# Optimization experiments

Measured on AMD Instinct MI355X. Metric: run time of the kernel, lower is better.

## Reference

```python
import jax, jax.numpy as jnp
import numpy as np

NUM_SENT, SENT_LEN, HIDDEN, OUT = 128, 64, 512, 512
N = NUM_SENT * SENT_LEN


def setup_inputs() -> dict:
    key = jax.random.key(0)
    ks = jax.random.split(key, 14)
    s = 1.0 / np.sqrt(HIDDEN)
    so = 1.0 / np.sqrt(OUT)
    return {
        "x": jax.random.normal(ks[0], (NUM_SENT, SENT_LEN, HIDDEN), jnp.float32),
        "mask": jax.random.uniform(ks[1], (N,), jnp.float32),
        "a_ud": jax.random.normal(ks[2], (N, N), jnp.float32) * 0.01,
        "a_lr": jax.random.normal(ks[3], (N, N), jnp.float32) * 0.01,
        "W": jax.random.uniform(ks[4], (OUT, HIDDEN), jnp.float32, -s, s),
        "b": jax.random.uniform(ks[5], (OUT,), jnp.float32, -s, s),
        "W_ud": jax.random.uniform(ks[6], (OUT, HIDDEN), jnp.float32, -s, s),
        "b_ud": jax.random.uniform(ks[7], (OUT,), jnp.float32, -s, s),
        "W_lr": jax.random.uniform(ks[8], (OUT, HIDDEN), jnp.float32, -s, s),
        "b_lr": jax.random.uniform(ks[9], (OUT,), jnp.float32, -s, s),
        "W_g": jax.random.uniform(ks[10], (OUT, HIDDEN), jnp.float32, -s, s),
        "b_g": jax.random.uniform(ks[11], (OUT,), jnp.float32, -s, s),
        "W_go": jax.random.uniform(ks[12], (OUT, OUT), jnp.float32, -so, so),
        "b_go": jax.random.uniform(ks[13], (OUT,), jnp.float32, -so, so),
    }


def reference(x, mask, a_ud, a_lr, W, b, W_ud, b_ud, W_lr, b_lr, W_g, b_g, W_go, b_go):
    num_sent, sent_len, hidden = x.shape
    xf = x.reshape(-1, hidden)                       # [N, H]
    h_ud = a_ud @ xf                                 # [N, H] neighbor aggregation (up/down)
    h_lr = a_lr @ xf                                 # [N, H] neighbor aggregation (left/right)
    h = (xf @ W.T + b) + (h_ud @ W_ud.T + b_ud) + (h_lr @ W_lr.T + b_lr)  # [N, OUT]
    # global node branch: masked mean-pool of relu(linear_g(x))
    n = mask.sum()
    h_g = (mask[None, :] @ jax.nn.relu(xf @ W_g.T + b_g)) / n  # [1, OUT]
    h = h + (h_g @ W_go.T + b_go)                    # broadcast add over N rows
    h = jax.nn.relu(h).reshape(num_sent, sent_len, -1)
    return (h, h_g)
```

## Files before the change

### kernel.cpp

```cpp
#include <hip/hip_runtime.h>
#include <stdint.h>


typedef __attribute__((ext_vector_type(8))) short short8;
typedef __attribute__((ext_vector_type(4))) float f32x4;

typedef const __attribute__((address_space(1))) void* gas1_t;
typedef __attribute__((address_space(3))) void* las3_t;

__device__ __forceinline__ void gload16(const void* g, void* l) {
  __builtin_amdgcn_global_load_lds((gas1_t)g, (las3_t)l, 16, 0, 0);
}

__device__ __forceinline__ unsigned pack2t(float lo, float hi) {
  return __builtin_amdgcn_perm(__float_as_uint(hi), __float_as_uint(lo), 0x07060302u);
}

__device__ __forceinline__ unsigned f2bf_rne(float f) {
  unsigned u = __float_as_uint(f);
  return (u + 0x7FFFu + ((u >> 16) & 1u)) >> 16;
}
__device__ __forceinline__ unsigned pack2_rne(float lo, float hi) {
  return f2bf_rne(lo) | (f2bf_rne(hi) << 16);
}

__global__ __launch_bounds__(256) void k1_convert(
    const float* __restrict__ x, const float* __restrict__ W,
    const float* __restrict__ W_ud, const float* __restrict__ W_lr,
    const float* __restrict__ W_g,
    uint16_t* __restrict__ xb, uint16_t* __restrict__ Yt, uint16_t* __restrict__ Wb1)
{
  unsigned tid = blockIdx.x * 256u + threadIdx.x;
  const float* src;
  uint16_t* dst;
  if (tid < 524288u) {
    src = x + (size_t)tid * 8;
    dst = xb + (size_t)tid * 8;
  } else {
    unsigned r = tid - 524288u;
    unsigned which = r >> 15;
    unsigned e8 = (r & 32767u) * 8;
    src = (which == 0 ? W : which == 1 ? W_ud : which == 2 ? W_lr : W_g) + e8;
    if (which == 0) {
      unsigned n = e8 >> 9, k = e8 & 511u;
      dst = Yt + (size_t)n * 16896 + 16384 + k;
    } else {
      dst = Wb1 + (size_t)(which - 1) * 262144 + e8;
    }
  }
  float4 v0 = ((const float4*)src)[0];
  float4 v1 = ((const float4*)src)[1];
  uint4 p;
  p.x = pack2_rne(v0.x, v0.y); p.y = pack2_rne(v0.z, v0.w);
  p.z = pack2_rne(v1.x, v1.y); p.w = pack2_rne(v1.z, v1.w);
  *(uint4*)dst = p;
}

__global__ __launch_bounds__(256) void k2_gemm1(
    const uint16_t* __restrict__ xb, const uint16_t* __restrict__ Wb1,
    const float* __restrict__ mask, const float* __restrict__ b_g,
    uint16_t* __restrict__ Yt, float* __restrict__ colsum)
{
  __shared__ __align__(16) char smem[34816];
  char* const bufA = smem;
  char* const bufB = smem + 8192;

  const int t = threadIdx.x;
  const int i0 = blockIdx.x * 128;
  const int bn = blockIdx.y;
  const int n0 = bn * 128;
  const int lane = t & 63, w = t >> 6;
  const int q = lane >> 4, l15 = lane & 15;
  const int wm = w >> 1, wn = w & 1;
  const int srow = t >> 2, spart = t & 3;

  f32x4 acc[4][4] = {};

  const uint16_t* const aA0 = xb + (size_t)(i0 + srow) * 512 + spart * 8;
  const uint16_t* const aA1 = aA0 + (size_t)64 * 512;
  const uint16_t* const aB0 = Wb1 + (size_t)(n0 + srow) * 512 + spart * 8;
  const uint16_t* const aB1 = aB0 + (size_t)64 * 512;

  for (int s = 0; s < 16; ++s) {
    __syncthreads();
    const int kk = s << 5;
    gload16(aA0 + kk, bufA + t * 16);
    gload16(aA1 + kk, bufA + 4096 + t * 16);
    gload16(aB0 + kk, bufB + t * 16);
    gload16(aB1 + kk, bufB + 4096 + t * 16);
    __syncthreads();
    short8 af[4], bf[4];
#pragma unroll
    for (int mi = 0; mi < 4; ++mi)
      af[mi] = *(const short8*)(bufA + (wm * 64 + mi * 16 + l15) * 64 + q * 16);
#pragma unroll
    for (int ni = 0; ni < 4; ++ni)
      bf[ni] = *(const short8*)(bufB + (wn * 64 + ni * 16 + l15) * 64 + q * 16);
#pragma unroll
    for (int mi = 0; mi < 4; ++mi)
#pragma unroll
      for (int ni = 0; ni < 4; ++ni)
        acc[mi][ni] = __builtin_amdgcn_mfma_f32_16x16x32_bf16(af[mi], bf[ni], acc[mi][ni], 0, 0, 0);
  }
  __syncthreads();

  const int g = bn >> 2;
  const int jb = (bn & 3) * 128;

  if (g < 2) {
    uint16_t* T = (uint16_t*)smem;
#pragma unroll
    for (int mi = 0; mi < 4; ++mi) {
#pragma unroll
      for (int ni = 0; ni < 4; ++ni) {
        int jl = wn * 64 + ni * 16 + l15;
#pragma unroll
        for (int r = 0; r < 4; ++r) {
          int il = wm * 64 + mi * 16 + q * 4 + r;
          T[jl * 136 + il] = (uint16_t)f2bf_rne(acc[mi][ni][r]);
        }
      }
    }
    __syncthreads();
    const int jl = t >> 1, half = t & 1;
    uint16_t* dst = Yt + (size_t)(jb + jl) * 16896 + (size_t)g * 8192 + i0 + half * 64;
    const uint16_t* srcT = T + jl * 136 + half * 64;
#pragma unroll
    for (int c = 0; c < 8; ++c)
      *(uint4*)(dst + c * 8) = *(const uint4*)(srcT + c * 8);
  } else {
    float mk[4][4];
#pragma unroll
    for (int mi = 0; mi < 4; ++mi)
#pragma unroll
      for (int r = 0; r < 4; ++r)
        mk[mi][r] = mask[i0 + wm * 64 + mi * 16 + q * 4 + r];
#pragma unroll
    for (int ni = 0; ni < 4; ++ni) {
      const int jl = jb + wn * 64 + ni * 16 + l15;
      const float bg = b_g[jl];
      float p = 0.f;
#pragma unroll
      for (int mi = 0; mi < 4; ++mi)
#pragma unroll
        for (int r = 0; r < 4; ++r)
          p += fmaxf(acc[mi][ni][r] + bg, 0.f) * mk[mi][r];
      p += __shfl_xor(p, 16);
      p += __shfl_xor(p, 32);
      if (q == 0) atomicAdd(&colsum[jl], p);
    }
  }
}

__global__ __launch_bounds__(256) void k4_finalize(
    const float* __restrict__ colsum, const float* __restrict__ mask,
    const float* __restrict__ b, const float* __restrict__ b_ud,
    const float* __restrict__ b_lr, const float* __restrict__ W_go,
    const float* __restrict__ b_go,
    float* __restrict__ row_add, float* __restrict__ out_hg)
{
  __shared__ float red[256];
  __shared__ float hg[512];
  const int t = threadIdx.x;
  float s = 0.f;
  for (int k = t; k < 8192; k += 256) s += mask[k];
  red[t] = s;
  __syncthreads();
  for (int o = 128; o > 0; o >>= 1) {
    if (t < o) red[t] += red[t + o];
    __syncthreads();
  }
  const float n = red[0];
  for (int j = t; j < 512; j += 256) hg[j] = colsum[j] / n;
  __syncthreads();

  const int j0 = blockIdx.x * 64;
  const int jj = j0 + (t >> 2);
  const int seg = t & 3;
  const float4* wrow = (const float4*)(W_go + (size_t)jj * 512 + seg * 128);
  float p = 0.f;
#pragma unroll 4
  for (int c = 0; c < 32; ++c) {
    float4 wv = wrow[c];
    const float* h4 = &hg[seg * 128 + c * 4];
    p += wv.x * h4[0] + wv.y * h4[1] + wv.z * h4[2] + wv.w * h4[3];
  }
  p += __shfl_down(p, 2);
  p += __shfl_down(p, 1);
  if ((t & 3) == 0)
    row_add[jj] = b[jj] + b_ud[jj] + b_lr[jj] + b_go[jj] + p;
  if (t < 64) out_hg[j0 + t] = hg[j0 + t];
}

__global__ __launch_bounds__(256, 4) void k5_gemm_big(
    const float* __restrict__ a_ud, const float* __restrict__ a_lr,
    const float* __restrict__ x, const uint16_t* __restrict__ Yt,
    float* __restrict__ out, float* __restrict__ P, int nsteps)
{
  __shared__ __align__(16) char smem[34816];
  char* const A0 = smem;
  char* const A1 = smem + 9216;
  char* const B0 = smem + 18432;
  char* const B1 = smem + 26624;

  const int t = threadIdx.x;
  const int i0 = blockIdx.x * 128;
  const int j0 = blockIdx.y * 128;
  const int z  = blockIdx.z;
  const int lane = t & 63;
  const int q = lane >> 4, l15 = lane & 15;
  const int w = t >> 6;
  const int wm = w >> 1, wn = w & 1;

  const int arow = t >> 1, ahalf = t & 1;
  const int brow = t >> 2;
  const int bchunk = (t & 3) ^ ((t >> 3) & 3);

  f32x4 acc[4][4] = {};
  const int kbase0 = z * (nsteps << 5);

  float4 av0, av1, av2, av3;
#define A_SRC(gk) ((gk) < 8192 \
    ? a_ud + (size_t)(i0 + arow) * 8192 + (gk) + ahalf * 16 \
    : ((gk) < 16384 \
      ? a_lr + (size_t)(i0 + arow) * 8192 + ((gk) - 8192) + ahalf * 16 \
      : x + (size_t)(i0 + arow) * 512 + ((gk) - 16384) + ahalf * 16))

  {
    const float* as = A_SRC(kbase0);
    av0 = ((const float4*)as)[0]; av1 = ((const float4*)as)[1];
    av2 = ((const float4*)as)[2]; av3 = ((const float4*)as)[3];
#pragma unroll
    for (int r = 0; r < 2; ++r)
      gload16(Yt + (size_t)(j0 + brow + r * 64) * 16896 + kbase0 + bchunk * 8,
              B0 + r * 4096 + t * 16);
    uint4 p0, p1;
    p0.x = pack2t(av0.x, av0.y); p0.y = pack2t(av0.z, av0.w);
    p0.z = pack2t(av1.x, av1.y); p0.w = pack2t(av1.z, av1.w);
    p1.x = pack2t(av2.x, av2.y); p1.y = pack2t(av2.z, av2.w);
    p1.z = pack2t(av3.x, av3.y); p1.w = pack2t(av3.z, av3.w);
    *(uint4*)(A0 + arow * 72 + ahalf * 32) = p0;
    *(uint4*)(A0 + arow * 72 + ahalf * 32 + 16) = p1;
  }

  for (int s = 0; s < nsteps; ++s) {
    __syncthreads();
    const bool more = (s + 1 < nsteps);
    char* const cA = (s & 1) ? A1 : A0;
    char* const cB = (s & 1) ? B1 : B0;
    char* const nA = (s & 1) ? A0 : A1;
    char* const nB = (s & 1) ? B0 : B1;

    if (more) {
      const int gk = kbase0 + ((s + 1) << 5);
      const float* as = A_SRC(gk);
      av0 = ((const float4*)as)[0]; av1 = ((const float4*)as)[1];
      av2 = ((const float4*)as)[2]; av3 = ((const float4*)as)[3];
#pragma unroll
      for (int r = 0; r < 2; ++r)
        gload16(Yt + (size_t)(j0 + brow + r * 64) * 16896 + gk + bchunk * 8,
                nB + r * 4096 + t * 16);
    }

    short8 af[4], bf[4];
#pragma unroll
    for (int mi = 0; mi < 4; ++mi)
      af[mi] = *(const short8*)(cA + (wm * 64 + mi * 16 + l15) * 72 + q * 16);
#pragma unroll
    for (int ni = 0; ni < 4; ++ni) {
      const int j = wn * 64 + ni * 16 + l15;
      bf[ni] = *(const short8*)(cB + j * 64 + ((q ^ ((j >> 1) & 3)) * 16));
    }
#pragma unroll
    for (int mi = 0; mi < 4; ++mi)
#pragma unroll
      for (int ni = 0; ni < 4; ++ni)
        acc[mi][ni] = __builtin_amdgcn_mfma_f32_16x16x32_bf16(af[mi], bf[ni], acc[mi][ni], 0, 0, 0);

    if (more) {
      uint4 p0, p1;
      p0.x = pack2t(av0.x, av0.y); p0.y = pack2t(av0.z, av0.w);
      p0.z = pack2t(av1.x, av1.y); p0.w = pack2t(av1.z, av1.w);
      p1.x = pack2t(av2.x, av2.y); p1.y = pack2t(av2.z, av2.w);
      p1.z = pack2t(av3.x, av3.y); p1.w = pack2t(av3.z, av3.w);
      *(uint4*)(nA + arow * 72 + ahalf * 32) = p0;
      *(uint4*)(nA + arow * 72 + ahalf * 32 + 16) = p1;
    }
  }
#undef A_SRC

  float* dst = z ? P + (size_t)(z - 1) * 4194304 : out;
#pragma unroll
  for (int ni = 0; ni < 4; ++ni) {
    const int jl = j0 + wn * 64 + ni * 16 + l15;
#pragma unroll
    for (int mi = 0; mi < 4; ++mi)
#pragma unroll
      for (int r = 0; r < 4; ++r) {
        const int il = i0 + wm * 64 + mi * 16 + q * 4 + r;
        dst[(size_t)il * 512 + jl] = acc[mi][ni][r];
      }
  }
}

__global__ __launch_bounds__(256) void k6_combine(
    const float* __restrict__ P, const float* __restrict__ row_add,
    float* __restrict__ out, int npart)
{
  const int idx = blockIdx.x * 256 + threadIdx.x;
  float4 a = ((const float4*)out)[idx];
  for (int p = 0; p < npart; ++p) {
    const float4 v = ((const float4*)P)[(size_t)p * 1048576 + idx];
    a.x += v.x; a.y += v.y; a.z += v.z; a.w += v.w;
  }
  const float4 r = ((const float4*)row_add)[idx & 127];
  float4 o;
  o.x = fmaxf(a.x + r.x, 0.f);
  o.y = fmaxf(a.y + r.y, 0.f);
  o.z = fmaxf(a.z + r.z, 0.f);
  o.w = fmaxf(a.w + r.w, 0.f);
  ((float4*)out)[idx] = o;
}

extern "C" void kernel_launch(void* const* d_in, const int* in_sizes, int n_in,
                              void* d_out, int out_size, void* d_ws, size_t ws_size,
                              hipStream_t stream) {
  (void)in_sizes; (void)n_in; (void)out_size;
  const float* x    = (const float*)d_in[0];
  const float* mask = (const float*)d_in[1];
  const float* a_ud = (const float*)d_in[2];
  const float* a_lr = (const float*)d_in[3];
  const float* W    = (const float*)d_in[4];
  const float* b    = (const float*)d_in[5];
  const float* W_ud = (const float*)d_in[6];
  const float* b_ud = (const float*)d_in[7];
  const float* W_lr = (const float*)d_in[8];
  const float* b_lr = (const float*)d_in[9];
  const float* W_g  = (const float*)d_in[10];
  const float* b_g  = (const float*)d_in[11];
  const float* W_go = (const float*)d_in[12];
  const float* b_go = (const float*)d_in[13];
  float* out = (float*)d_out;

  char* ws = (char*)d_ws;
  uint16_t* xb     = (uint16_t*)(ws);
  uint16_t* Yt     = (uint16_t*)(ws + 8388608);
  uint16_t* Wb1    = (uint16_t*)(ws + 25690112);
  float*    colsum = (float*)(ws + 27262976);
  float*    rowadd = (float*)(ws + 27265024);
  float*    P      = (float*)(ws + 27267072);

  const int Z = (ws_size >= 77598720u) ? 4 : 2;
  const int nsteps = (16896 / Z) / 32;

  hipMemsetAsync(colsum, 0, 512 * sizeof(float), stream);
  k1_convert<<<2560, 256, 0, stream>>>(x, W, W_ud, W_lr, W_g, xb, Yt, Wb1);
  k2_gemm1<<<dim3(64, 12), 256, 0, stream>>>(xb, Wb1, mask, b_g, Yt, colsum);
  k4_finalize<<<8, 256, 0, stream>>>(colsum, mask, b, b_ud, b_lr, W_go, b_go,
                                     rowadd, out + 4194304);
  k5_gemm_big<<<dim3(64, 4, Z), 256, 0, stream>>>(a_ud, a_lr, x, Yt, out, P, nsteps);
  k6_combine<<<4096, 256, 0, stream>>>(P, rowadd, out, Z - 1);
}
```

Measured before the change: 863.0 us.

## Double-buffer gemm1 with swizzled LDS and deepen big-GEMM A prefetch to two stages

In the first GEMM kernel, tiles are now double-buffered in LDS and prefetched one step ahead. An XOR swizzle on the chunk index is meant to cut LDS bank conflicts, and one barrier per step is removed. In the big GEMM, the fp32 A operand now loads two steps ahead into alternating register sets, with explicit vmcnt waits and sched_barriers replacing __syncthreads, to hide global latency more deeply. The big GEMM's occupancy hint drops from 4 to 3 blocks per SIMD to allow the extra registers. This loses some latency hiding from fewer resident waves, and the hand-written waitcnt counts must match the number of outstanding loads exactly.

```diff
diff --git a/kernel.cpp b/kernel.cpp
--- a/kernel.cpp
+++ b/kernel.cpp
@@ -62,8 +62,10 @@
     uint16_t* __restrict__ Yt, float* __restrict__ colsum)
 {
   __shared__ __align__(16) char smem[34816];
-  char* const bufA = smem;
-  char* const bufB = smem + 8192;
+  char* const A0 = smem;
+  char* const B0 = smem + 8192;
+  char* const A1 = smem + 16384;
+  char* const B1 = smem + 24576;
 
   const int t = threadIdx.x;
   const int i0 = blockIdx.x * 128;
@@ -72,30 +74,45 @@
   const int lane = t & 63, w = t >> 6;
   const int q = lane >> 4, l15 = lane & 15;
   const int wm = w >> 1, wn = w & 1;
-  const int srow = t >> 2, spart = t & 3;
+  const int srow = t >> 2;
+  const int sw = (t & 3) ^ ((srow >> 1) & 3);
 
   f32x4 acc[4][4] = {};
 
-  const uint16_t* const aA0 = xb + (size_t)(i0 + srow) * 512 + spart * 8;
+  const uint16_t* const aA0 = xb + (size_t)(i0 + srow) * 512 + sw * 8;
   const uint16_t* const aA1 = aA0 + (size_t)64 * 512;
-  const uint16_t* const aB0 = Wb1 + (size_t)(n0 + srow) * 512 + spart * 8;
+  const uint16_t* const aB0 = Wb1 + (size_t)(n0 + srow) * 512 + sw * 8;
   const uint16_t* const aB1 = aB0 + (size_t)64 * 512;
+
+  gload16(aA0, A0 + t * 16);
+  gload16(aA1, A0 + 4096 + t * 16);
+  gload16(aB0, B0 + t * 16);
+  gload16(aB1, B0 + 4096 + t * 16);
 
   for (int s = 0; s < 16; ++s) {
     __syncthreads();
-    const int kk = s << 5;
-    gload16(aA0 + kk, bufA + t * 16);
-    gload16(aA1 + kk, bufA + 4096 + t * 16);
-    gload16(aB0 + kk, bufB + t * 16);
-    gload16(aB1 + kk, bufB + 4096 + t * 16);
-    __syncthreads();
+    if (s < 15) {
+      const int kk = (s + 1) << 5;
+      char* const nA = (s & 1) ? A0 : A1;
+      char* const nB = (s & 1) ? B0 : B1;
+      gload16(aA0 + kk, nA + t * 16);
+      gload16(aA1 + kk, nA + 4096 + t * 16);
+      gload16(aB0 + kk, nB + t * 16);
+      gload16(aB1 + kk, nB + 4096 + t * 16);
+    }
+    char* const cA = (s & 1) ? A1 : A0;
+    char* const cB = (s & 1) ? B1 : B0;
     short8 af[4], bf[4];
 #pragma unroll
-    for (int mi = 0; mi < 4; ++mi)
-      af[mi] = *(const short8*)(bufA + (wm * 64 + mi * 16 + l15) * 64 + q * 16);
-#pragma unroll
-    for (int ni = 0; ni < 4; ++ni)
-      bf[ni] = *(const short8*)(bufB + (wn * 64 + ni * 16 + l15) * 64 + q * 16);
+    for (int mi = 0; mi < 4; ++mi) {
+      const int r = wm * 64 + mi * 16 + l15;
+      af[mi] = *(const short8*)(cA + r * 64 + ((q ^ ((r >> 1) & 3)) * 16));
+    }
+#pragma unroll
+    for (int ni = 0; ni < 4; ++ni) {
+      const int r = wn * 64 + ni * 16 + l15;
+      bf[ni] = *(const short8*)(cB + r * 64 + ((q ^ ((r >> 1) & 3)) * 16));
+    }
 #pragma unroll
     for (int mi = 0; mi < 4; ++mi)
 #pragma unroll
@@ -192,7 +209,7 @@
   if (t < 64) out_hg[j0 + t] = hg[j0 + t];
 }
 
-__global__ __launch_bounds__(256, 4) void k5_gemm_big(
+__global__ __launch_bounds__(256, 3) void k5_gemm_big(
     const float* __restrict__ a_ud, const float* __restrict__ a_lr,
     const float* __restrict__ x, const uint16_t* __restrict__ Yt,
     float* __restrict__ out, float* __restrict__ P, int nsteps)
@@ -219,74 +236,86 @@
   f32x4 acc[4][4] = {};
   const int kbase0 = z * (nsteps << 5);
 
-  float4 av0, av1, av2, av3;
+  float4 aX0, aX1, aX2, aX3, aY0, aY1, aY2, aY3;
+
 #define A_SRC(gk) ((gk) < 8192 \
     ? a_ud + (size_t)(i0 + arow) * 8192 + (gk) + ahalf * 16 \
     : ((gk) < 16384 \
       ? a_lr + (size_t)(i0 + arow) * 8192 + ((gk) - 8192) + ahalf * 16 \
       : x + (size_t)(i0 + arow) * 512 + ((gk) - 16384) + ahalf * 16))
 
-  {
-    const float* as = A_SRC(kbase0);
-    av0 = ((const float4*)as)[0]; av1 = ((const float4*)as)[1];
-    av2 = ((const float4*)as)[2]; av3 = ((const float4*)as)[3];
-#pragma unroll
-    for (int r = 0; r < 2; ++r)
-      gload16(Yt + (size_t)(j0 + brow + r * 64) * 16896 + kbase0 + bchunk * 8,
-              B0 + r * 4096 + t * 16);
-    uint4 p0, p1;
-    p0.x = pack2t(av0.x, av0.y); p0.y = pack2t(av0.z, av0.w);
-    p0.z = pack2t(av1.x, av1.y); p0.w = pack2t(av1.z, av1.w);
-    p1.x = pack2t(av2.x, av2.y); p1.y = pack2t(av2.z, av2.w);
-    p1.z = pack2t(av3.x, av3.y); p1.w = pack2t(av3.z, av3.w);
-    *(uint4*)(A0 + arow * 72 + ahalf * 32) = p0;
-    *(uint4*)(A0 + arow * 72 + ahalf * 32 + 16) = p1;
-  }
-
-  for (int s = 0; s < nsteps; ++s) {
-    __syncthreads();
-    const bool more = (s + 1 < nsteps);
-    char* const cA = (s & 1) ? A1 : A0;
-    char* const cB = (s & 1) ? B1 : B0;
-    char* const nA = (s & 1) ? A0 : A1;
-    char* const nB = (s & 1) ? B0 : B1;
-
-    if (more) {
-      const int gk = kbase0 + ((s + 1) << 5);
-      const float* as = A_SRC(gk);
-      av0 = ((const float4*)as)[0]; av1 = ((const float4*)as)[1];
-      av2 = ((const float4*)as)[2]; av3 = ((const float4*)as)[3];
-#pragma unroll
-      for (int r = 0; r < 2; ++r)
-        gload16(Yt + (size_t)(j0 + brow + r * 64) * 16896 + gk + bchunk * 8,
-                nB + r * 4096 + t * 16);
-    }
-
-    short8 af[4], bf[4];
-#pragma unroll
-    for (int mi = 0; mi < 4; ++mi)
-      af[mi] = *(const short8*)(cA + (wm * 64 + mi * 16 + l15) * 72 + q * 16);
-#pragma unroll
-    for (int ni = 0; ni < 4; ++ni) {
-      const int j = wn * 64 + ni * 16 + l15;
-      bf[ni] = *(const short8*)(cB + j * 64 + ((q ^ ((j >> 1) & 3)) * 16));
-    }
-#pragma unroll
-    for (int mi = 0; mi < 4; ++mi)
-#pragma unroll
-      for (int ni = 0; ni < 4; ++ni)
-        acc[mi][ni] = __builtin_amdgcn_mfma_f32_16x16x32_bf16(af[mi], bf[ni], acc[mi][ni], 0, 0, 0);
-
-    if (more) {
-      uint4 p0, p1;
-      p0.x = pack2t(av0.x, av0.y); p0.y = pack2t(av0.z, av0.w);
-      p0.z = pack2t(av1.x, av1.y); p0.w = pack2t(av1.z, av1.w);
-      p1.x = pack2t(av2.x, av2.y); p1.y = pack2t(av2.z, av2.w);
-      p1.z = pack2t(av3.x, av3.y); p1.w = pack2t(av3.z, av3.w);
-      *(uint4*)(nA + arow * 72 + ahalf * 32) = p0;
-      *(uint4*)(nA + arow * 72 + ahalf * 32 + 16) = p1;
-    }
-  }
+#define LOAD_A(R0, R1, R2, R3, gk) { \
+    const float* as_ = A_SRC(gk); \
+    R0 = ((const float4*)as_)[0]; R1 = ((const float4*)as_)[1]; \
+    R2 = ((const float4*)as_)[2]; R3 = ((const float4*)as_)[3]; }
+
+#define LOAD_B(dstB, gk) { \
+    gload16(Yt + (size_t)(j0 + brow) * 16896 + (gk) + bchunk * 8, (dstB) + t * 16); \
+    gload16(Yt + (size_t)(j0 + brow + 64) * 16896 + (gk) + bchunk * 8, (dstB) + 4096 + t * 16); }
+
+#define PACK_A(dstA, R0, R1, R2, R3) { \
+    uint4 p0_, p1_; \
+    p0_.x = pack2t(R0.x, R0.y); p0_.y = pack2t(R0.z, R0.w); \
+    p0_.z = pack2t(R1.x, R1.y); p0_.w = pack2t(R1.z, R1.w); \
+    p1_.x = pack2t(R2.x, R2.y); p1_.y = pack2t(R2.z, R2.w); \
+    p1_.z = pack2t(R3.x, R3.y); p1_.w = pack2t(R3.z, R3.w); \
+    *(uint4*)((dstA) + arow * 72 + ahalf * 32) = p0_; \
+    *(uint4*)((dstA) + arow * 72 + ahalf * 32 + 16) = p1_; }
+
+  LOAD_A(aX0, aX1, aX2, aX3, kbase0);
+  __builtin_amdgcn_sched_barrier(0);
+  LOAD_B(B0, kbase0);
+  __builtin_amdgcn_sched_barrier(0);
+  LOAD_A(aY0, aY1, aY2, aY3, kbase0 + 32);
+  __builtin_amdgcn_sched_barrier(0);
+  PACK_A(A0, aX0, aX1, aX2, aX3);
+  asm volatile("s_waitcnt vmcnt(4) lgkmcnt(0)" ::: "memory");
+  __builtin_amdgcn_sched_barrier(0);
+  __builtin_amdgcn_s_barrier();
+  __builtin_amdgcn_sched_barrier(0);
+
+#define K5_BODY(s_, LX0, LX1, LX2, LX3, PX0, PX1, PX2, PX3) { \
+    const int s__ = (s_); \
+    char* const cA_ = (s__ & 1) ? A1 : A0; \
+    char* const cB_ = (s__ & 1) ? B1 : B0; \
+    char* const nA_ = (s__ & 1) ? A0 : A1; \
+    char* const nB_ = (s__ & 1) ? B0 : B1; \
+    const bool h1_ = (s__ + 1 < nsteps); \
+    const bool h2_ = (s__ + 2 < nsteps); \
+    if (h1_) { LOAD_B(nB_, kbase0 + ((s__ + 1) << 5)); } \
+    __builtin_amdgcn_sched_barrier(0); \
+    if (h2_) { LOAD_A(LX0, LX1, LX2, LX3, kbase0 + ((s__ + 2) << 5)); } \
+    __builtin_amdgcn_sched_barrier(0); \
+    short8 af_[4], bf_[4]; \
+    _Pragma("unroll") \
+    for (int mi_ = 0; mi_ < 4; ++mi_) \
+      af_[mi_] = *(const short8*)(cA_ + (wm * 64 + mi_ * 16 + l15) * 72 + q * 16); \
+    _Pragma("unroll") \
+    for (int ni_ = 0; ni_ < 4; ++ni_) { \
+      const int j_ = wn * 64 + ni_ * 16 + l15; \
+      bf_[ni_] = *(const short8*)(cB_ + j_ * 64 + ((q ^ ((j_ >> 1) & 3)) * 16)); \
+    } \
+    _Pragma("unroll") \
+    for (int mi_ = 0; mi_ < 4; ++mi_) \
+      _Pragma("unroll") \
+      for (int ni_ = 0; ni_ < 4; ++ni_) \
+        acc[mi_][ni_] = __builtin_amdgcn_mfma_f32_16x16x32_bf16(af_[mi_], bf_[ni_], acc[mi_][ni_], 0, 0, 0); \
+    if (h1_) { PACK_A(nA_, PX0, PX1, PX2, PX3); } \
+    if (h2_) { asm volatile("s_waitcnt vmcnt(4) lgkmcnt(0)" ::: "memory"); } \
+    else     { asm volatile("s_waitcnt vmcnt(0) lgkmcnt(0)" ::: "memory"); } \
+    __builtin_amdgcn_sched_barrier(0); \
+    __builtin_amdgcn_s_barrier(); \
+    __builtin_amdgcn_sched_barrier(0); \
+  }
+
+  for (int s = 0; s < nsteps; s += 2) {
+    K5_BODY(s,     aX0, aX1, aX2, aX3, aY0, aY1, aY2, aY3);
+    K5_BODY(s + 1, aY0, aY1, aY2, aY3, aX0, aX1, aX2, aX3);
+  }
+#undef K5_BODY
+#undef PACK_A
+#undef LOAD_B
+#undef LOAD_A
 #undef A_SRC
 
   float* dst = z ? P + (size_t)(z - 1) * 4194304 : out;
```

New measurement: 931.6 us. 1.08x slower.
